# Optimization experiments

Hardware: AMD Instinct MI355X
Metric: run time of the kernel (lower is better)

The kernel has to match this reference:

```python
import jax, jax.numpy as jnp
import numpy as np

B, S, D = 2, 2048, 2048
QH, KVH, HD = 32, 8, 64
GRP = QH // KVH  # GQA group size = 4


def setup_inputs() -> dict:
    key = jax.random.key(0)
    ks = jax.random.split(key, 9)
    x = jax.random.normal(ks[0], (B, S, D), jnp.float32)
    # RoPE angle table: [S, HD//2] -> stacked (cos, sin) -> [S, HD//2, 2]
    inv_freq = 1.0 / (10000.0 ** (np.arange(0, HD, 2, dtype=np.float32) / HD))
    ang = np.arange(S, dtype=np.float32)[:, None] * inv_freq[None, :]
    freqs = jnp.stack([jnp.cos(jnp.asarray(ang)), jnp.sin(jnp.asarray(ang))], axis=-1).astype(jnp.float32)
    w = 0.02
    Wq = jax.random.normal(ks[1], (D, QH * HD), jnp.float32) * w
    bq = jnp.zeros((QH * HD,), jnp.float32)
    Wk = jax.random.normal(ks[2], (D, KVH * HD), jnp.float32) * w
    bk = jnp.zeros((KVH * HD,), jnp.float32)
    Wv = jax.random.normal(ks[3], (D, KVH * HD), jnp.float32) * w
    bv = jnp.zeros((KVH * HD,), jnp.float32)
    Wo = jax.random.normal(ks[4], (QH * HD, D), jnp.float32) * w
    bo = jnp.zeros((D,), jnp.float32)
    return {"x": x, "freqs": freqs, "Wq": Wq, "bq": bq, "Wk": Wk, "bk": bk,
            "Wv": Wv, "bv": bv, "Wo": Wo, "bo": bo}


def _rope(xh, cos, sin):
    # xh: [b, s, h, hd]; complex rotation on adjacent pairs, like view_as_complex
    b, s, h, hd = xh.shape
    xp = xh.reshape(b, s, h, hd // 2, 2)
    x0, x1 = xp[..., 0], xp[..., 1]
    o0 = x0 * cos - x1 * sin
    o1 = x0 * sin + x1 * cos
    return jnp.stack([o0, o1], axis=-1).reshape(b, s, h, hd)


def reference(x, freqs, Wq, bq, Wk, bk, Wv, bv, Wo, bo):
    b, s, _ = x.shape
    q = (x @ Wq + bq).reshape(b, s, QH, HD)
    k = (x @ Wk + bk).reshape(b, s, KVH, HD)
    v = (x @ Wv + bv).reshape(b, s, KVH, HD)
    cos = freqs[:s, :, 0][None, :, None, :]  # [1, s, 1, hd//2]
    sin = freqs[:s, :, 1][None, :, None, :]
    q = _rope(q, cos, sin)
    k = _rope(k, cos, sin)
    # [b, h, s, hd]
    q = q.transpose(0, 2, 1, 3).reshape(b, KVH, GRP, s, HD)
    k = k.transpose(0, 2, 1, 3)  # [b, kvh, s, hd]
    v = v.transpose(0, 2, 1, 3)
    scores = jnp.einsum('bkgsh,bkth->bkgst', q, k) / jnp.sqrt(jnp.float32(HD))
    attn = jax.nn.softmax(scores, axis=-1)
    o = jnp.einsum('bkgst,bkth->bkgsh', attn, v)  # [b, kvh, grp, s, hd]
    o = o.reshape(b, QH, s, HD).transpose(0, 2, 1, 3).reshape(b, s, QH * HD)
    return o @ Wo + bo
```

## Files before the change

kernel.cpp:

```cpp
#include <hip/hip_runtime.h>
#include <stdint.h>

#define B_   2
#define S_   2048
#define D_   2048
#define QH_  32
#define KVH_ 8
#define HD_  64

typedef short  short8  __attribute__((ext_vector_type(8)));
typedef float  floatx4 __attribute__((ext_vector_type(4)));

__device__ __forceinline__ ushort f2b(float f) {
  union { float f; uint32_t u; } c; c.f = f;
  uint32_t u = c.u;
  return (ushort)((u + 0x7FFFu + ((u >> 16) & 1u)) >> 16);
}

__device__ __forceinline__ uint32_t fbits(float f) {
  union { float f; uint32_t u; } c; c.f = f;
  return c.u;
}

__device__ __forceinline__ void dma16(const void* g, void* l) {
  __builtin_amdgcn_global_load_lds(
      (const __attribute__((address_space(1))) uint32_t*)(uintptr_t)g,
      (__attribute__((address_space(3))) uint32_t*)(uintptr_t)l, 16, 0, 0);
}


__global__ __launch_bounds__(256) void conv_x_kernel(const float* __restrict__ X,
                                                     ushort* __restrict__ Xb) {
  size_t i = ((size_t)blockIdx.x * 256 + threadIdx.x) * 4;
  float4 v = *(const float4*)(X + i);
  ushort4 o;
  o.x = f2b(v.x); o.y = f2b(v.y); o.z = f2b(v.z); o.w = f2b(v.w);
  *(ushort4*)(Xb + i) = o;
}

__global__ void tconv_kernel(const float* __restrict__ W, ushort* __restrict__ Wt,
                             int K, int N) {
  __shared__ float tile[32][33];
  int bx = blockIdx.x, by = blockIdx.y;
  int tx = threadIdx.x, ty = threadIdx.y;
#pragma unroll
  for (int i = 0; i < 32; i += 8)
    tile[ty + i][tx] = W[(size_t)(by * 32 + ty + i) * N + bx * 32 + tx];
  __syncthreads();
#pragma unroll
  for (int i = 0; i < 32; i += 8)
    Wt[(size_t)(bx * 32 + ty + i) * K + by * 32 + tx] = f2b(tile[tx][ty + i]);
}

__global__ void bias_kernel(const float* __restrict__ bq, const float* __restrict__ bk,
                            const float* __restrict__ bv, float* __restrict__ outb) {
  int i = blockIdx.x * 256 + threadIdx.x;
  if (i >= 3072) return;
  float v;
  if (i < 2048)      v = bq[i];
  else if (i < 2560) v = bk[i - 2048];
  else               v = bv[i - 2560];
  outb[i] = v;
}


__global__ __launch_bounds__(256) void gemm_bt_kernel(
    const ushort* __restrict__ A, const ushort* __restrict__ Bt,
    const float* __restrict__ bias, float* __restrict__ C,
    int M, int N, int K) {
  __shared__ ushort sA[2][128 * 32];
  __shared__ ushort sB[2][128 * 32];
  const int tid  = threadIdx.x;
  const int bm   = blockIdx.y, bn = blockIdx.x;
  const int wave = tid >> 6, lane = tid & 63;
  const int quad = lane >> 4, l16 = lane & 15;
  const int wm   = (wave >> 1) * 64, wn = (wave & 1) * 64;

  const ushort* Ab = A  + (size_t)(bm * 128) * K;
  const ushort* Bb = Bt + (size_t)(bn * 128) * K;

  const int gr = lane >> 2;
  const int gu = (lane & 3) * 8;

  floatx4 acc[4][4];
#pragma unroll
  for (int i = 0; i < 4; i++)
#pragma unroll
    for (int j = 0; j < 4; j++) acc[i][j] = (floatx4){0.f, 0.f, 0.f, 0.f};

#pragma unroll
  for (int j = 0; j < 2; j++) {
    int row = j * 64 + wave * 16 + gr;
    dma16(Ab + (size_t)row * K + gu, &sA[0][j * 2048 + wave * 512]);
    dma16(Bb + (size_t)row * K + gu, &sB[0][j * 2048 + wave * 512]);
  }

  int cur = 0;
  for (int k0 = 0; k0 < K; k0 += 32) {
    __syncthreads();
    if (k0 + 32 < K) {
      int nxt = cur ^ 1;
#pragma unroll
      for (int j = 0; j < 2; j++) {
        int row = j * 64 + wave * 16 + gr;
        dma16(Ab + (size_t)row * K + k0 + 32 + gu, &sA[nxt][j * 2048 + wave * 512]);
        dma16(Bb + (size_t)row * K + k0 + 32 + gu, &sB[nxt][j * 2048 + wave * 512]);
      }
    }
    short8 af[4], bf[4];
#pragma unroll
    for (int mi = 0; mi < 4; mi++)
      af[mi] = *(const short8*)&sA[cur][(wm + mi * 16 + l16) * 32 + quad * 8];
#pragma unroll
    for (int ni = 0; ni < 4; ni++)
      bf[ni] = *(const short8*)&sB[cur][(wn + ni * 16 + l16) * 32 + quad * 8];
#pragma unroll
    for (int mi = 0; mi < 4; mi++)
#pragma unroll
      for (int ni = 0; ni < 4; ni++)
        acc[mi][ni] = __builtin_amdgcn_mfma_f32_16x16x32_bf16(
            af[mi], bf[ni], acc[mi][ni], 0, 0, 0);
    cur ^= 1;
  }

#pragma unroll
  for (int mi = 0; mi < 4; mi++) {
#pragma unroll
    for (int ni = 0; ni < 4; ni++) {
      int col  = bn * 128 + wn + ni * 16 + l16;
      float bv = bias[col];
#pragma unroll
      for (int r = 0; r < 4; r++) {
        int row = bm * 128 + wm + mi * 16 + quad * 4 + r;
        C[(size_t)row * N + col] = acc[mi][ni][r] + bv;
      }
    }
  }
}


#define QSCALE 0.18033688f

__global__ __launch_bounds__(256) void rope_qk_kernel(
    const float* __restrict__ QKVf, const float* __restrict__ freqs,
    ushort* __restrict__ Qb, ushort* __restrict__ Kb) {
  int idx = blockIdx.x * 256 + threadIdx.x;
  int row = idx / 1280;
  int pc  = idx - row * 1280;
  int col = pc * 2;
  int b = row >> 11, s = row & 2047;
  const float* p = QKVf + (size_t)row * 3072 + col;
  float x0 = p[0], x1 = p[1];
  int hp = (col >> 1) & 31;
  float2 cs = ((const float2*)freqs)[s * 32 + hp];
  float o0 = x0 * cs.x - x1 * cs.y;
  float o1 = x0 * cs.y + x1 * cs.x;
  if (col < 2048) {
    o0 *= QSCALE; o1 *= QSCALE;
    uint32_t pack = (uint32_t)f2b(o0) | ((uint32_t)f2b(o1) << 16);
    int h = col >> 6, d = col & 63;
    *(uint32_t*)&Qb[(((size_t)(b * QH_ + h)) * S_ + s) * HD_ + d] = pack;
  } else {
    int cc = col - 2048;
    int h = cc >> 6, d = cc & 63;
    uint32_t pack = (uint32_t)f2b(o0) | ((uint32_t)f2b(o1) << 16);
    *(uint32_t*)&Kb[(((size_t)(b * KVH_ + h)) * S_ + s) * HD_ + d] = pack;
  }
}


__global__ void vpack_kernel(const float* __restrict__ QKVf, ushort* __restrict__ Vt) {
  __shared__ ushort tile[64][65];
  int s0 = blockIdx.x * 64;
  int bh = blockIdx.y;
  int tx = threadIdx.x, ty = threadIdx.y;
  int vcol = 2560 + (bh & 7) * 64;
  int brow = (bh >> 3) * S_;
#pragma unroll
  for (int i = 0; i < 64; i += 8)
    tile[ty + i][tx] = f2b(QKVf[(size_t)(brow + s0 + ty + i) * 3072 + vcol + tx]);
  __syncthreads();
  int pt = (tx & 15) * 4 + (tx >> 4);
#pragma unroll
  for (int i = 0; i < 64; i += 8)
    Vt[((size_t)bh * HD_ + ty + i) * S_ + s0 + pt] = tile[tx][ty + i];
}


__global__ __launch_bounds__(512, 4) void attn_kernel(
    const ushort* __restrict__ Q, const ushort* __restrict__ K,
    const ushort* __restrict__ Vt, ushort* __restrict__ O) {
  const int qt = blockIdx.x, qh = blockIdx.y, b = blockIdx.z;
  const int kvh = qh >> 2;
  const int tid = threadIdx.x;
  const int wave = tid >> 6, lane = tid & 63;
  const int quad = lane >> 4, l16 = lane & 15;

  __shared__ ushort kBuf[2][64 * 64];
  __shared__ ushort vBuf[2][64 * 64];
  __shared__ ushort P[8][16 * 72];

  const ushort* Qh = Q  + ((size_t)(b * QH_ + qh)) * S_ * HD_;
  const ushort* Kh = K  + ((size_t)(b * KVH_ + kvh)) * S_ * HD_;
  const ushort* Vh = Vt + ((size_t)(b * KVH_ + kvh)) * HD_ * S_;

  const int dr = lane >> 3;
  const int du = (lane & 7) ^ (dr & 7);
  const size_t kLaneOff = (size_t)(wave * 8 + dr) * 64 + du * 8;
  const size_t vLaneOff = (size_t)(wave * 8 + dr) * S_ + du * 8;
  const int swz = (l16 & 7);

  const int q0 = qt * 256 + wave * 32;
  short8 aq[2][2];
#pragma unroll
  for (int m = 0; m < 2; m++)
#pragma unroll
    for (int s2 = 0; s2 < 2; s2++)
      aq[m][s2] = *(const short8*)(Qh + (size_t)(q0 + m * 16 + l16) * HD_ + s2 * 32 + quad * 8);

  floatx4 oacc[2][4];
#pragma unroll
  for (int m = 0; m < 2; m++)
#pragma unroll
    for (int t = 0; t < 4; t++) oacc[m][t] = (floatx4){0.f, 0.f, 0.f, 0.f};
  float ls[2][4] = {{0.f, 0.f, 0.f, 0.f}, {0.f, 0.f, 0.f, 0.f}};

  dma16(Kh + kLaneOff, &kBuf[0][wave * 512]);
  dma16(Vh + vLaneOff, &vBuf[0][wave * 512]);

  int cur = 0;
  for (int kv0 = 0; kv0 < S_; kv0 += 64) {
    __syncthreads();
    if (kv0 + 64 < S_) {
      int nxt = cur ^ 1;
      dma16(Kh + (size_t)(kv0 + 64) * 64 + kLaneOff, &kBuf[nxt][wave * 512]);
      dma16(Vh + (size_t)(kv0 + 64) + vLaneOff,      &vBuf[nxt][wave * 512]);
    }

    short8 kf[4][2];
#pragma unroll
    for (int c = 0; c < 4; c++)
#pragma unroll
      for (int s2 = 0; s2 < 2; s2++)
        kf[c][s2] = *(const short8*)&kBuf[cur][(c * 16 + l16) * 64 + (((s2 * 4 + quad) ^ swz) * 8)];

#pragma unroll
    for (int m = 0; m < 2; m++) {
      floatx4 sc[4];
#pragma unroll
      for (int c = 0; c < 4; c++) sc[c] = (floatx4){0.f, 0.f, 0.f, 0.f};
#pragma unroll
      for (int c = 0; c < 4; c++)
#pragma unroll
        for (int s2 = 0; s2 < 2; s2++)
          sc[c] = __builtin_amdgcn_mfma_f32_16x16x32_bf16(aq[m][s2], kf[c][s2], sc[c], 0, 0, 0);

#pragma unroll
      for (int r = 0; r < 4; r++) {
        float p0 = __builtin_amdgcn_exp2f(sc[0][r]);
        float p1 = __builtin_amdgcn_exp2f(sc[1][r]);
        float p2 = __builtin_amdgcn_exp2f(sc[2][r]);
        float p3 = __builtin_amdgcn_exp2f(sc[3][r]);
        ls[m][r] += (p0 + p1) + (p2 + p3);
        uint2 u;
        u.x = __builtin_amdgcn_perm(fbits(p1) + 0x8000u, fbits(p0) + 0x8000u, 0x07060302u);
        u.y = __builtin_amdgcn_perm(fbits(p3) + 0x8000u, fbits(p2) + 0x8000u, 0x07060302u);
        *(uint2*)&P[wave][(quad * 4 + r) * 72 + l16 * 4] = u;
      }

#pragma unroll
      for (int s2 = 0; s2 < 2; s2++) {
        short8 ap = *(const short8*)&P[wave][l16 * 72 + s2 * 32 + quad * 8];
#pragma unroll
        for (int t = 0; t < 4; t++) {
          short8 bv = *(const short8*)&vBuf[cur][(t * 16 + l16) * 64 + (((s2 * 4 + quad) ^ swz) * 8)];
          oacc[m][t] = __builtin_amdgcn_mfma_f32_16x16x32_bf16(ap, bv, oacc[m][t], 0, 0, 0);
        }
      }
    }
    cur ^= 1;
  }

#pragma unroll
  for (int m = 0; m < 2; m++) {
#pragma unroll
    for (int r = 0; r < 4; r++) {
      float l = ls[m][r];
#pragma unroll
      for (int st = 1; st < 16; st <<= 1) l += __shfl_xor(l, st, 16);
      float inv = 1.0f / l;
      int srow = q0 + m * 16 + quad * 4 + r;
      size_t base = ((size_t)b * S_ + srow) * (QH_ * HD_) + (size_t)qh * HD_;
#pragma unroll
      for (int t = 0; t < 4; t++)
        O[base + t * 16 + l16] = f2b(oacc[m][t][r] * inv);
    }
  }
}


extern "C" void kernel_launch(void* const* d_in, const int* in_sizes, int n_in,
                              void* d_out, int out_size, void* d_ws, size_t ws_size,
                              hipStream_t stream) {
  const float* x  = (const float*)d_in[0];
  const float* fr = (const float*)d_in[1];
  const float* Wq = (const float*)d_in[2];
  const float* bq = (const float*)d_in[3];
  const float* Wk = (const float*)d_in[4];
  const float* bk = (const float*)d_in[5];
  const float* Wv = (const float*)d_in[6];
  const float* bv = (const float*)d_in[7];
  const float* Wo = (const float*)d_in[8];
  const float* bo = (const float*)d_in[9];
  float* out = (float*)d_out;
  char* ws = (char*)d_ws;

  ushort* xb    = (ushort*)(ws + 0);
  ushort* wqkv  = (ushort*)(ws + 16777216);
  ushort* wo    = (ushort*)(ws + 29360128);
  float*  biasq = (float* )(ws + 37748736);
  float*  qkvf  = (float* )(ws + 37761024);
  ushort* qb    = (ushort*)(ws + 88092672);
  ushort* kb    = (ushort*)(ws + 104869888);
  ushort* vt    = (ushort*)(ws + 109064192);
  ushort* ob    = xb;

  conv_x_kernel<<<8192, 256, 0, stream>>>(x, xb);
  dim3 tb(32, 8);
  tconv_kernel<<<dim3(2048 / 32, 2048 / 32), tb, 0, stream>>>(Wq, wqkv, 2048, 2048);
  tconv_kernel<<<dim3(512 / 32, 2048 / 32), tb, 0, stream>>>(Wk, wqkv + (size_t)2048 * 2048, 2048, 512);
  tconv_kernel<<<dim3(512 / 32, 2048 / 32), tb, 0, stream>>>(Wv, wqkv + (size_t)2560 * 2048, 2048, 512);
  tconv_kernel<<<dim3(2048 / 32, 2048 / 32), tb, 0, stream>>>(Wo, wo, 2048, 2048);
  bias_kernel<<<12, 256, 0, stream>>>(bq, bk, bv, biasq);

  gemm_bt_kernel<<<dim3(3072 / 128, 4096 / 128), 256, 0, stream>>>(
      xb, wqkv, biasq, qkvf, 4096, 3072, 2048);

  rope_qk_kernel<<<20480, 256, 0, stream>>>(qkvf, fr, qb, kb);
  vpack_kernel<<<dim3(2048 / 64, 16), dim3(64, 8), 0, stream>>>(qkvf, vt);

  attn_kernel<<<dim3(8, 32, 2), 512, 0, stream>>>(qb, kb, vt, ob);

  gemm_bt_kernel<<<dim3(2048 / 128, 4096 / 128), 256, 0, stream>>>(
      ob, wo, bo, out, 4096, 2048, 2048);
}
```

Before: 347.3 us.

## Fuse RoPE and head-major bf16 packing into QKV GEMM epilogue

A dedicated QKV GEMM now applies bias, RoPE (pair exchange via lane shuffle), Q scaling and bf16 conversion in its epilogue. It writes Q, K and V directly in head-major layout, so the fp32 QKV buffer and the separate rope kernel are no longer needed. The four weight transpose launches are merged into one launch. In attention, V fragments are hoisted out of the m loop into registers so they are loaded once per tile, at the cost of more register pressure. The epilogue issues scattered 2-byte stores, which may be less efficient than the old packed stores.

```diff
diff --git a/kernel.cpp b/kernel.cpp
--- a/kernel.cpp
+++ b/kernel.cpp
@@ -27,6 +27,8 @@
       (const __attribute__((address_space(1))) uint32_t*)(uintptr_t)g,
       (__attribute__((address_space(3))) uint32_t*)(uintptr_t)l, 16, 0, 0);
 }
+
+#define QSCALE 0.18033688f
 
 
 __global__ __launch_bounds__(256) void conv_x_kernel(const float* __restrict__ X,
@@ -38,10 +40,18 @@
   *(ushort4*)(Xb + i) = o;
 }
 
-__global__ void tconv_kernel(const float* __restrict__ W, ushort* __restrict__ Wt,
-                             int K, int N) {
+__global__ void tconv_all_kernel(const float* __restrict__ Wq, const float* __restrict__ Wk,
+                                 const float* __restrict__ Wv, const float* __restrict__ Wo,
+                                 ushort* __restrict__ wqkv, ushort* __restrict__ wo) {
   __shared__ float tile[32][33];
+  int z = blockIdx.z;
+  const float* W; ushort* Wt; int N;
+  if (z == 0)      { W = Wq; Wt = wqkv;                        N = 2048; }
+  else if (z == 1) { W = Wk; Wt = wqkv + (size_t)2048 * 2048;  N = 512;  }
+  else if (z == 2) { W = Wv; Wt = wqkv + (size_t)2560 * 2048;  N = 512;  }
+  else             { W = Wo; Wt = wo;                          N = 2048; }
   int bx = blockIdx.x, by = blockIdx.y;
+  if (bx * 32 >= N) return;
   int tx = threadIdx.x, ty = threadIdx.y;
 #pragma unroll
   for (int i = 0; i < 32; i += 8)
@@ -49,7 +59,7 @@
   __syncthreads();
 #pragma unroll
   for (int i = 0; i < 32; i += 8)
-    Wt[(size_t)(bx * 32 + ty + i) * K + by * 32 + tx] = f2b(tile[tx][ty + i]);
+    Wt[(size_t)(bx * 32 + ty + i) * 2048 + by * 32 + tx] = f2b(tile[tx][ty + i]);
 }
 
 __global__ void bias_kernel(const float* __restrict__ bq, const float* __restrict__ bk,
@@ -61,6 +71,106 @@
   else if (i < 2560) v = bk[i - 2048];
   else               v = bv[i - 2560];
   outb[i] = v;
+}
+
+
+__global__ __launch_bounds__(256) void gemm_qkv_kernel(
+    const ushort* __restrict__ A, const ushort* __restrict__ Bt,
+    const float* __restrict__ bias, const float2* __restrict__ F2,
+    ushort* __restrict__ qb, ushort* __restrict__ kb, ushort* __restrict__ vb) {
+  const int K = 2048;
+  __shared__ ushort sA[2][128 * 32];
+  __shared__ ushort sB[2][128 * 32];
+  const int tid  = threadIdx.x;
+  const int bm   = blockIdx.y, bn = blockIdx.x;
+  const int wave = tid >> 6, lane = tid & 63;
+  const int quad = lane >> 4, l16 = lane & 15;
+  const int wm   = (wave >> 1) * 64, wn = (wave & 1) * 64;
+
+  const ushort* Ab = A  + (size_t)(bm * 128) * K;
+  const ushort* Bb = Bt + (size_t)(bn * 128) * K;
+
+  const int gr = lane >> 2;
+  const int gu = (lane & 3) * 8;
+
+  floatx4 acc[4][4];
+#pragma unroll
+  for (int i = 0; i < 4; i++)
+#pragma unroll
+    for (int j = 0; j < 4; j++) acc[i][j] = (floatx4){0.f, 0.f, 0.f, 0.f};
+
+#pragma unroll
+  for (int j = 0; j < 2; j++) {
+    int row = j * 64 + wave * 16 + gr;
+    dma16(Ab + (size_t)row * K + gu, &sA[0][j * 2048 + wave * 512]);
+    dma16(Bb + (size_t)row * K + gu, &sB[0][j * 2048 + wave * 512]);
+  }
+
+  int cur = 0;
+  for (int k0 = 0; k0 < K; k0 += 32) {
+    __syncthreads();
+    if (k0 + 32 < K) {
+      int nxt = cur ^ 1;
+#pragma unroll
+      for (int j = 0; j < 2; j++) {
+        int row = j * 64 + wave * 16 + gr;
+        dma16(Ab + (size_t)row * K + k0 + 32 + gu, &sA[nxt][j * 2048 + wave * 512]);
+        dma16(Bb + (size_t)row * K + k0 + 32 + gu, &sB[nxt][j * 2048 + wave * 512]);
+      }
+    }
+    short8 af[4], bf[4];
+#pragma unroll
+    for (int mi = 0; mi < 4; mi++)
+      af[mi] = *(const short8*)&sA[cur][(wm + mi * 16 + l16) * 32 + quad * 8];
+#pragma unroll
+    for (int ni = 0; ni < 4; ni++)
+      bf[ni] = *(const short8*)&sB[cur][(wn + ni * 16 + l16) * 32 + quad * 8];
+#pragma unroll
+    for (int mi = 0; mi < 4; mi++)
+#pragma unroll
+      for (int ni = 0; ni < 4; ni++)
+        acc[mi][ni] = __builtin_amdgcn_mfma_f32_16x16x32_bf16(
+            af[mi], bf[ni], acc[mi][ni], 0, 0, 0);
+    cur ^= 1;
+  }
+
+  const int isQ = (bn < 16);
+  const int isV = (bn >= 20);
+  const int hh  = wn >> 6;
+  const float sySign = (l16 & 1) ? 1.f : -1.f;
+  ushort* dst;
+  int hbase;
+  if (isQ)      { dst = qb; hbase = bn * 2 + hh; }
+  else if (!isV){ dst = kb; hbase = (bn - 16) * 2 + hh; }
+  else          { dst = vb; hbase = (bn - 20) * 2 + hh; }
+  const int NH = isQ ? QH_ : KVH_;
+
+#pragma unroll
+  for (int mi = 0; mi < 4; mi++) {
+#pragma unroll
+    for (int ni = 0; ni < 4; ni++) {
+      int col = bn * 128 + wn + ni * 16 + l16;
+      float bvv = bias[col];
+      int d  = (wn + ni * 16 + l16) & 63;
+      int hp = (((wn + ni * 16) >> 1) + (l16 >> 1)) & 31;
+#pragma unroll
+      for (int r = 0; r < 4; r++) {
+        int row = bm * 128 + wm + mi * 16 + quad * 4 + r;
+        int s = row & 2047, bb = row >> 11;
+        float xv = acc[mi][ni][r] + bvv;
+        size_t base = (((size_t)bb * NH + hbase) * S_ + s) * HD_ + d;
+        if (!isV) {
+          float2 cs = F2[s * 32 + hp];
+          float pp = __shfl_xor(xv, 1);
+          float o = fmaf(pp * sySign, cs.y, xv * cs.x);
+          if (isQ) o *= QSCALE;
+          dst[base] = f2b(o);
+        } else {
+          dst[base] = f2b(xv);
+        }
+      }
+    }
+  }
 }
 
 
@@ -139,46 +249,14 @@
 }
 
 
-#define QSCALE 0.18033688f
-
-__global__ __launch_bounds__(256) void rope_qk_kernel(
-    const float* __restrict__ QKVf, const float* __restrict__ freqs,
-    ushort* __restrict__ Qb, ushort* __restrict__ Kb) {
-  int idx = blockIdx.x * 256 + threadIdx.x;
-  int row = idx / 1280;
-  int pc  = idx - row * 1280;
-  int col = pc * 2;
-  int b = row >> 11, s = row & 2047;
-  const float* p = QKVf + (size_t)row * 3072 + col;
-  float x0 = p[0], x1 = p[1];
-  int hp = (col >> 1) & 31;
-  float2 cs = ((const float2*)freqs)[s * 32 + hp];
-  float o0 = x0 * cs.x - x1 * cs.y;
-  float o1 = x0 * cs.y + x1 * cs.x;
-  if (col < 2048) {
-    o0 *= QSCALE; o1 *= QSCALE;
-    uint32_t pack = (uint32_t)f2b(o0) | ((uint32_t)f2b(o1) << 16);
-    int h = col >> 6, d = col & 63;
-    *(uint32_t*)&Qb[(((size_t)(b * QH_ + h)) * S_ + s) * HD_ + d] = pack;
-  } else {
-    int cc = col - 2048;
-    int h = cc >> 6, d = cc & 63;
-    uint32_t pack = (uint32_t)f2b(o0) | ((uint32_t)f2b(o1) << 16);
-    *(uint32_t*)&Kb[(((size_t)(b * KVH_ + h)) * S_ + s) * HD_ + d] = pack;
-  }
-}
-
-
-__global__ void vpack_kernel(const float* __restrict__ QKVf, ushort* __restrict__ Vt) {
+__global__ void vpack_kernel(const ushort* __restrict__ vb, ushort* __restrict__ Vt) {
   __shared__ ushort tile[64][65];
   int s0 = blockIdx.x * 64;
   int bh = blockIdx.y;
   int tx = threadIdx.x, ty = threadIdx.y;
-  int vcol = 2560 + (bh & 7) * 64;
-  int brow = (bh >> 3) * S_;
 #pragma unroll
   for (int i = 0; i < 64; i += 8)
-    tile[ty + i][tx] = f2b(QKVf[(size_t)(brow + s0 + ty + i) * 3072 + vcol + tx]);
+    tile[ty + i][tx] = vb[((size_t)bh * S_ + s0 + ty + i) * HD_ + tx];
   __syncthreads();
   int pt = (tx & 15) * 4 + (tx >> 4);
 #pragma unroll
@@ -237,12 +315,17 @@
       dma16(Vh + (size_t)(kv0 + 64) + vLaneOff,      &vBuf[nxt][wave * 512]);
     }
 
-    short8 kf[4][2];
+    short8 kf[4][2], vf[2][4];
 #pragma unroll
     for (int c = 0; c < 4; c++)
 #pragma unroll
       for (int s2 = 0; s2 < 2; s2++)
         kf[c][s2] = *(const short8*)&kBuf[cur][(c * 16 + l16) * 64 + (((s2 * 4 + quad) ^ swz) * 8)];
+#pragma unroll
+    for (int s2 = 0; s2 < 2; s2++)
+#pragma unroll
+      for (int t = 0; t < 4; t++)
+        vf[s2][t] = *(const short8*)&vBuf[cur][(t * 16 + l16) * 64 + (((s2 * 4 + quad) ^ swz) * 8)];
 
 #pragma unroll
     for (int m = 0; m < 2; m++) {
@@ -272,10 +355,8 @@
       for (int s2 = 0; s2 < 2; s2++) {
         short8 ap = *(const short8*)&P[wave][l16 * 72 + s2 * 32 + quad * 8];
 #pragma unroll
-        for (int t = 0; t < 4; t++) {
-          short8 bv = *(const short8*)&vBuf[cur][(t * 16 + l16) * 64 + (((s2 * 4 + quad) ^ swz) * 8)];
-          oacc[m][t] = __builtin_amdgcn_mfma_f32_16x16x32_bf16(ap, bv, oacc[m][t], 0, 0, 0);
-        }
+        for (int t = 0; t < 4; t++)
+          oacc[m][t] = __builtin_amdgcn_mfma_f32_16x16x32_bf16(ap, vf[s2][t], oacc[m][t], 0, 0, 0);
       }
     }
     cur ^= 1;
@@ -319,25 +400,20 @@
   ushort* wqkv  = (ushort*)(ws + 16777216);
   ushort* wo    = (ushort*)(ws + 29360128);
   float*  biasq = (float* )(ws + 37748736);
-  float*  qkvf  = (float* )(ws + 37761024);
-  ushort* qb    = (ushort*)(ws + 88092672);
-  ushort* kb    = (ushort*)(ws + 104869888);
-  ushort* vt    = (ushort*)(ws + 109064192);
+  ushort* qb    = (ushort*)(ws + 37761024);
+  ushort* kb    = (ushort*)(ws + 54538240);
+  ushort* vb    = (ushort*)(ws + 58732544);
+  ushort* vt    = (ushort*)(ws + 62926848);
   ushort* ob    = xb;
 
   conv_x_kernel<<<8192, 256, 0, stream>>>(x, xb);
-  dim3 tb(32, 8);
-  tconv_kernel<<<dim3(2048 / 32, 2048 / 32), tb, 0, stream>>>(Wq, wqkv, 2048, 2048);
-  tconv_kernel<<<dim3(512 / 32, 2048 / 32), tb, 0, stream>>>(Wk, wqkv + (size_t)2048 * 2048, 2048, 512);
-  tconv_kernel<<<dim3(512 / 32, 2048 / 32), tb, 0, stream>>>(Wv, wqkv + (size_t)2560 * 2048, 2048, 512);
-  tconv_kernel<<<dim3(2048 / 32, 2048 / 32), tb, 0, stream>>>(Wo, wo, 2048, 2048);
+  tconv_all_kernel<<<dim3(64, 64, 4), dim3(32, 8), 0, stream>>>(Wq, Wk, Wv, Wo, wqkv, wo);
   bias_kernel<<<12, 256, 0, stream>>>(bq, bk, bv, biasq);
 
-  gemm_bt_kernel<<<dim3(3072 / 128, 4096 / 128), 256, 0, stream>>>(
-      xb, wqkv, biasq, qkvf, 4096, 3072, 2048);
-
-  rope_qk_kernel<<<20480, 256, 0, stream>>>(qkvf, fr, qb, kb);
-  vpack_kernel<<<dim3(2048 / 64, 16), dim3(64, 8), 0, stream>>>(qkvf, vt);
+  gemm_qkv_kernel<<<dim3(3072 / 128, 4096 / 128), 256, 0, stream>>>(
+      xb, wqkv, biasq, (const float2*)fr, qb, kb, vb);
+
+  vpack_kernel<<<dim3(2048 / 64, 16), dim3(64, 8), 0, stream>>>(vb, vt);
 
   attn_kernel<<<dim3(8, 32, 2), 512, 0, stream>>>(qb, kb, vt, ob);
 
```

After: 379.1 us. 9.2% more time.
